# Kernel tuning notes

Hardware: AMD Instinct MI355X
Metric: run time of the kernel (lower is better)

The kernel has to match this reference:

```python
import jax, jax.numpy as jnp
import numpy as np

NUM_HEADS = 4
D_MODEL = 256
HEAD_DIM = D_MODEL // NUM_HEADS  # 64
B, N = 8, 2048


def _proj(x, W, b):
    # Conv1d with kernel_size=1 == pointwise linear over channel dim
    # x: [B, C_in, N], W: [C_out, C_in], b: [C_out]
    return jnp.einsum('oi,bin->bon', W, x) + b[None, :, None]


def setup_inputs() -> dict:
    key = jax.random.key(0)
    ks = jax.random.split(key, 11)
    s = 1.0 / np.sqrt(D_MODEL)
    return {
        'query': jax.random.normal(ks[0], (B, D_MODEL, N), jnp.float32),
        'key':   jax.random.normal(ks[1], (B, D_MODEL, N), jnp.float32),
        'value': jax.random.normal(ks[2], (B, D_MODEL, N), jnp.float32),
        'Wq': jax.random.normal(ks[3], (D_MODEL, D_MODEL), jnp.float32) * s,
        'bq': jax.random.normal(ks[4], (D_MODEL,), jnp.float32) * 0.01,
        'Wk': jax.random.normal(ks[5], (D_MODEL, D_MODEL), jnp.float32) * s,
        'bk': jax.random.normal(ks[6], (D_MODEL,), jnp.float32) * 0.01,
        'Wv': jax.random.normal(ks[7], (D_MODEL, D_MODEL), jnp.float32) * s,
        'bv': jax.random.normal(ks[8], (D_MODEL,), jnp.float32) * 0.01,
        'Wm': jax.random.normal(ks[9], (D_MODEL, D_MODEL), jnp.float32) * s,
        'bm': jax.random.normal(ks[10], (D_MODEL,), jnp.float32) * 0.01,
    }


def reference(query, key, value, Wq, bq, Wk, bk, Wv, bv, Wm, bm):
    b = query.shape[0]
    # project then split channels into (head_dim, num_heads): [B, d, h, N]
    q = _proj(query, Wq, bq).reshape(b, HEAD_DIM, NUM_HEADS, -1)
    k = _proj(key,   Wk, bk).reshape(b, HEAD_DIM, NUM_HEADS, -1)
    v = _proj(value, Wv, bv).reshape(b, HEAD_DIM, NUM_HEADS, -1)
    scale = 1.0 / jnp.sqrt(jnp.asarray(HEAD_DIM, q.dtype))
    scores = jnp.einsum('bdhn,bdhm->bhnm', q, k) * scale  # [B,H,N,N]
    prob = jax.nn.softmax(scores, axis=-1)
    x = jnp.einsum('bhnm,bdhm->bdhn', prob, v)  # [B,d,H,N]
    x = x.reshape(b, HEAD_DIM * NUM_HEADS, -1)  # [B, d_model, N]
    return _proj(x, Wm, bm)
```

## Files before the change

### kernel.cpp

```cpp
#include <hip/hip_runtime.h>
#include <math.h>


constexpr int BATCH  = 8;
constexpr int DMODEL = 256;
constexpr int SEQ    = 2048;
constexpr int HDIM   = 64;
constexpr int TN     = 128;
constexpr int TM     = 64;
constexpr int NJT    = SEQ / TM;

typedef _Float16 half4_t __attribute__((ext_vector_type(4)));
typedef _Float16 half8_t __attribute__((ext_vector_type(8)));
typedef float    float4_t __attribute__((ext_vector_type(4)));

static __device__ __forceinline__ void ld16_lds(const void* g, void* l) {
    __builtin_amdgcn_global_load_lds(
        (const __attribute__((address_space(1))) unsigned*)g,
        (__attribute__((address_space(3))) unsigned*)l, 16, 0, 0);
}

__global__ __launch_bounds__(256)
void prep_w(const float* __restrict__ Wq, const float* __restrict__ Wk,
            const float* __restrict__ Wv, const float* __restrict__ Wm,
            _Float16* __restrict__ wf)
{
    const int which = blockIdx.y;
    const float* src = which == 0 ? Wq : which == 1 ? Wk : which == 2 ? Wv : Wm;
    const int i = (blockIdx.x * 256 + threadIdx.x) * 4;
    const float4 v = *(const float4*)&src[i];
    half4_t o; o[0] = v.x; o[1] = v.y; o[2] = v.z; o[3] = v.w;
    *(half4_t*)&wf[(size_t)which * DMODEL * DMODEL + i] = o;
}

__global__ __launch_bounds__(256, 3)
void gemm_qkv(const _Float16* __restrict__ wf, const float* __restrict__ bq,
              const float* __restrict__ bk, const float* __restrict__ bv,
              const float* __restrict__ Xq, const float* __restrict__ Xk,
              const float* __restrict__ Xv, _Float16* __restrict__ qT,
              _Float16* __restrict__ kT, _Float16* __restrict__ vT)
{
    const int n0 = blockIdx.x * 64;
    const int proj = blockIdx.y >> 3, b = blockIdx.y & 7;
    const _Float16* W    = wf + (size_t)proj * DMODEL * DMODEL;
    const float*    bias = proj == 0 ? bq : proj == 1 ? bk : bv;
    const float*    X    = (proj == 0 ? Xq : proj == 1 ? Xk : Xv)
                           + (size_t)b * DMODEL * SEQ;

    __shared__ __align__(16) char lds[50432];
    float*    T  = (float*)lds;
    _Float16* Xs = (_Float16*)(lds + 16640);
    _Float16* Tw = (_Float16*)lds;

    const int tid = threadIdx.x, tn = tid & 15, tc = tid >> 4;

    #pragma unroll
    for (int cc = 0; cc < 4; ++cc) {
        __syncthreads();
        #pragma unroll
        for (int i = 0; i < 4; ++i) {
            const int c = tc + 16 * i;
            const float4 v = *(const float4*)&X[(size_t)(cc * 64 + c) * SEQ + n0 + tn * 4];
            T[c * 65 + tn * 4 + 0] = v.x; T[c * 65 + tn * 4 + 1] = v.y;
            T[c * 65 + tn * 4 + 2] = v.z; T[c * 65 + tn * 4 + 3] = v.w;
        }
        __syncthreads();
        #pragma unroll
        for (int i = 0; i < 4; ++i) {
            const int n = tc + 16 * i;
            half4_t h4;
            #pragma unroll
            for (int j = 0; j < 4; ++j) h4[j] = (_Float16)T[(tn * 4 + j) * 65 + n];
            *(half4_t*)&Xs[n * 264 + cc * 64 + tn * 4] = h4;
        }
    }
    __syncthreads();

    const int w = tid >> 6, lane = tid & 63;
    const int lm = lane & 15, g = lane >> 4, g8 = g * 8;
    const int cw0 = w * 64;

    float4_t acc[4][4];
    #pragma unroll
    for (int mt = 0; mt < 4; ++mt)
        #pragma unroll
        for (int nt = 0; nt < 4; ++nt) acc[mt][nt] = (float4_t){0.f, 0.f, 0.f, 0.f};

    #pragma unroll
    for (int k0 = 0; k0 < DMODEL; k0 += 64) {
        half8_t a[4][2], bb[4][2];
        #pragma unroll
        for (int mt = 0; mt < 4; ++mt)
            #pragma unroll
            for (int kd = 0; kd < 2; ++kd)
                a[mt][kd] = *(const half8_t*)&W[(size_t)(cw0 + mt * 16 + lm) * DMODEL
                                                + k0 + kd * 32 + g8];
        #pragma unroll
        for (int nt = 0; nt < 4; ++nt)
            #pragma unroll
            for (int kd = 0; kd < 2; ++kd)
                bb[nt][kd] = *(const half8_t*)&Xs[(nt * 16 + lm) * 264
                                                  + k0 + kd * 32 + g8];
        #pragma unroll
        for (int kd = 0; kd < 2; ++kd)
            #pragma unroll
            for (int mt = 0; mt < 4; ++mt)
                #pragma unroll
                for (int nt = 0; nt < 4; ++nt)
                    acc[mt][nt] = __builtin_amdgcn_mfma_f32_16x16x32_f16(
                        a[mt][kd], bb[nt][kd], acc[mt][nt], 0, 0, 0);
    }
    __syncthreads();

    #pragma unroll
    for (int mt = 0; mt < 4; ++mt) {
        const float4 b4 = *(const float4*)&bias[cw0 + mt * 16 + g * 4];
        const float bb4[4] = {b4.x, b4.y, b4.z, b4.w};
        #pragma unroll
        for (int nt = 0; nt < 4; ++nt) {
            half4_t pk;
            #pragma unroll
            for (int r = 0; r < 4; ++r) pk[r] = (_Float16)(acc[mt][nt][r] + bb4[r]);
            *(half4_t*)&Tw[((w * 64 + nt * 16 + lm)) * 68 + mt * 16 + g * 4] = pk;
        }
    }

    if (proj < 2) {
        _Float16* dst = (proj == 0 ? qT : kT);
        const int h2 = lane >> 4, lml = lane & 15;
        #pragma unroll
        for (int it = 0; it < 4; ++it) {
            const int nl = it * 16 + lml;
            #pragma unroll
            for (int dc = 0; dc < 2; ++dc) {
                half8_t ch;
                #pragma unroll
                for (int e = 0; e < 8; ++e)
                    ch[e] = Tw[(w * 64 + nl) * 68 + 4 * (dc * 8 + e) + h2];
                const int chunk = (w * 2 + dc) ^ (nl & 7);
                *(half8_t*)&dst[((size_t)(b * 4 + h2) * SEQ + n0 + nl) * HDIM
                                + chunk * 8] = ch;
            }
        }
    } else {
        const int hh = lane & 3, dl = (lane >> 2) & 15;
        const int d = w * 16 + dl;
        const size_t rowbase =
            (((size_t)(b * 4 + hh) * NJT + (n0 >> 6)) * HDIM + d) * (size_t)TM;
        #pragma unroll
        for (int jc = 0; jc < 8; ++jc) {
            half8_t ch;
            #pragma unroll
            for (int e = 0; e < 8; ++e)
                ch[e] = Tw[(w * 64 + jc * 8 + e) * 68 + 4 * dl + hh];
            *(half8_t*)&vT[rowbase + ((jc ^ (dl & 7)) << 3)] = ch;
        }
    }
}

__global__ __launch_bounds__(256, 4)
void attn_f16(const _Float16* __restrict__ qT, const _Float16* __restrict__ kT,
              const _Float16* __restrict__ vT, _Float16* __restrict__ xa,
              _Float16* __restrict__ xb, float* __restrict__ rs)
{
    const int bh = blockIdx.z, b = bh >> 2, h = bh & 3;
    const int jh = blockIdx.y;
    const int tid = threadIdx.x, wid = tid >> 6, lane = tid & 63;
    const int lm = lane & 15, g = lane >> 4;
    const int i0 = blockIdx.x * TN + wid * 32;

    __shared__ _Float16 Kb[2][TM * HDIM];
    __shared__ _Float16 Vb[2][TM * HDIM];

    half8_t bq[2][2];
    const _Float16* qbase = qT + (size_t)bh * SEQ * HDIM;
    #pragma unroll
    for (int rt = 0; rt < 2; ++rt)
        #pragma unroll
        for (int kd = 0; kd < 2; ++kd) {
            const int row = i0 + rt * 16 + lm;
            half8_t r8 = *(const half8_t*)(qbase + (size_t)row * HDIM
                                           + (((kd * 4 + g) ^ (lm & 7)) << 3));
            #pragma unroll
            for (int e = 0; e < 8; ++e) r8[e] = r8[e] * (_Float16)0.125f;
            bq[rt][kd] = r8;
        }

    const char* kt = (const char*)(kT + ((size_t)bh * SEQ + jh * (SEQ / 2)) * HDIM);
    const char* vt = (const char*)(vT + ((size_t)bh * NJT + jh * 16) * TM * HDIM);

    float4_t o[2][4], o5[2];
    #pragma unroll
    for (int rt = 0; rt < 2; ++rt) {
        #pragma unroll
        for (int dt = 0; dt < 4; ++dt) o[rt][dt] = (float4_t){0.f, 0.f, 0.f, 0.f};
        o5[rt] = (float4_t){0.f, 0.f, 0.f, 0.f};
    }
    const half4_t vone = {(_Float16)1.f, (_Float16)1.f, (_Float16)1.f, (_Float16)1.f};

    #define STAGE(jt, bu)                                                     \
        {                                                                     \
            const char* kg = kt + (size_t)(jt) * 8192;                        \
            const char* vg = vt + (size_t)(jt) * 8192;                        \
            _Pragma("unroll")                                                 \
            for (int p = 0; p < 2; ++p) {                                     \
                const int c = wid + p * 4;                                    \
                ld16_lds(kg + c * 1024 + lane * 16, (char*)&Kb[bu][0] + c * 1024); \
                ld16_lds(vg + c * 1024 + lane * 16, (char*)&Vb[bu][0] + c * 1024); \
            }                                                                 \
        }

    STAGE(0, 0);
    __syncthreads();

    for (int jt = 0; jt < 16; ++jt) {
        const int cur = jt & 1;
        if (jt + 1 < 16) STAGE(jt + 1, cur ^ 1);

        float4_t s[4][2];
        #pragma unroll
        for (int ct = 0; ct < 4; ++ct)
            #pragma unroll
            for (int rt = 0; rt < 2; ++rt) s[ct][rt] = (float4_t){0.f, 0.f, 0.f, 0.f};
        #pragma unroll
        for (int kd = 0; kd < 2; ++kd)
            #pragma unroll
            for (int ct = 0; ct < 4; ++ct) {
                const half8_t fk = *(const half8_t*)
                    &Kb[cur][(ct * 16 + lm) * HDIM + (((kd * 4 + g) ^ (lm & 7)) << 3)];
                #pragma unroll
                for (int rt = 0; rt < 2; ++rt)
                    s[ct][rt] = __builtin_amdgcn_mfma_f32_16x16x32_f16(
                        fk, bq[rt][kd], s[ct][rt], 0, 0, 0);
            }

        half4_t ap[4][2];
        #pragma unroll
        for (int ct = 0; ct < 4; ++ct)
            #pragma unroll
            for (int rt = 0; rt < 2; ++rt)
                #pragma unroll
                for (int r = 0; r < 4; ++r)
                    ap[ct][rt][r] = (_Float16)__expf(s[ct][rt][r]);
        #pragma unroll
        for (int ct = 0; ct < 4; ++ct)
            #pragma unroll
            for (int rt = 0; rt < 2; ++rt)
                o5[rt] = __builtin_amdgcn_mfma_f32_16x16x16f16(
                    ap[ct][rt], vone, o5[rt], 0, 0, 0);

        #pragma unroll
        for (int ct = 0; ct < 4; ++ct)
            #pragma unroll
            for (int dt = 0; dt < 4; ++dt) {
                const int d = dt * 16 + lm;
                const half4_t fv = *(const half4_t*)
                    &Vb[cur][d * TM + ((((ct * 2 + (g >> 1)) ^ (lm & 7)) << 3)
                                       + ((g & 1) << 2))];
                #pragma unroll
                for (int rt = 0; rt < 2; ++rt)
                    o[rt][dt] = __builtin_amdgcn_mfma_f32_16x16x16f16(
                        ap[ct][rt], fv, o[rt][dt], 0, 0, 0);
            }
        __syncthreads();
    }

    _Float16* xp = jh ? xb : xa;
    #pragma unroll
    for (int rt = 0; rt < 2; ++rt)
        #pragma unroll
        for (int dt = 0; dt < 4; ++dt) {
            const int c = 4 * (dt * 16 + lm) + h;
            #pragma unroll
            for (int r = 0; r < 4; ++r) {
                const int n = i0 + rt * 16 + 4 * g + r;
                xp[((size_t)b * SEQ + n) * DMODEL + c] = (_Float16)o[rt][dt][r];
            }
        }
    if (lm == 0) {
        #pragma unroll
        for (int rt = 0; rt < 2; ++rt)
            #pragma unroll
            for (int r = 0; r < 4; ++r)
                rs[((size_t)jh * 32 + bh) * SEQ + i0 + rt * 16 + 4 * g + r] =
                    o5[rt][r];
    }
    #undef STAGE
}

__global__ __launch_bounds__(256)
void gemm_final(const _Float16* __restrict__ wm, const float* __restrict__ bias,
                const _Float16* __restrict__ xa, const _Float16* __restrict__ xb,
                const float* __restrict__ rs, float* __restrict__ out)
{
    const int n0 = blockIdx.x * 64, m0 = blockIdx.y * 128;
    const int b = blockIdx.z;
    const int tid = threadIdx.x, w = tid >> 6, lane = tid & 63;
    const int lm = lane & 15, g = lane >> 4, g8 = g * 8;
    const int cw0 = m0 + w * 32;

    const _Float16* Xa = xa + ((size_t)b * SEQ + n0) * DMODEL;
    const _Float16* Xb2 = xb + ((size_t)b * SEQ + n0) * DMODEL;

    half8_t pm[4];
    #pragma unroll
    for (int nt = 0; nt < 4; ++nt) {
        const int n = n0 + nt * 16 + lm;
        #pragma unroll
        for (int hh = 0; hh < 4; ++hh) {
            const float l = rs[(size_t)(b * 4 + hh) * SEQ + n]
                          + rs[(size_t)(32 + b * 4 + hh) * SEQ + n];
            const _Float16 iv = (_Float16)(1.0f / l);
            pm[nt][hh] = iv; pm[nt][hh + 4] = iv;
        }
    }

    float4_t acc[2][4];
    #pragma unroll
    for (int mt = 0; mt < 2; ++mt)
        #pragma unroll
        for (int nt = 0; nt < 4; ++nt) acc[mt][nt] = (float4_t){0.f, 0.f, 0.f, 0.f};

    #pragma unroll
    for (int k0 = 0; k0 < DMODEL; k0 += 64) {
        half8_t a[2][2], bb[4][2];
        #pragma unroll
        for (int mt = 0; mt < 2; ++mt)
            #pragma unroll
            for (int kd = 0; kd < 2; ++kd)
                a[mt][kd] = *(const half8_t*)&wm[(size_t)(cw0 + mt * 16 + lm) * DMODEL
                                                 + k0 + kd * 32 + g8];
        #pragma unroll
        for (int nt = 0; nt < 4; ++nt)
            #pragma unroll
            for (int kd = 0; kd < 2; ++kd) {
                const size_t off = (size_t)(nt * 16 + lm) * DMODEL + k0 + kd * 32 + g8;
                const half8_t va = *(const half8_t*)&Xa[off];
                const half8_t vb = *(const half8_t*)&Xb2[off];
                bb[nt][kd] = (va + vb) * pm[nt];
            }
        #pragma unroll
        for (int kd = 0; kd < 2; ++kd)
            #pragma unroll
            for (int mt = 0; mt < 2; ++mt)
                #pragma unroll
                for (int nt = 0; nt < 4; ++nt)
                    acc[mt][nt] = __builtin_amdgcn_mfma_f32_16x16x32_f16(
                        a[mt][kd], bb[nt][kd], acc[mt][nt], 0, 0, 0);
    }

    #pragma unroll
    for (int mt = 0; mt < 2; ++mt)
        #pragma unroll
        for (int r = 0; r < 4; ++r) {
            const int co = cw0 + mt * 16 + g * 4 + r;
            const float bv_ = bias[co];
            #pragma unroll
            for (int nt = 0; nt < 4; ++nt)
                out[((size_t)b * DMODEL + co) * SEQ + n0 + nt * 16 + lm] =
                    acc[mt][nt][r] + bv_;
        }
}

extern "C" void kernel_launch(void* const* d_in, const int* in_sizes, int n_in,
                              void* d_out, int out_size, void* d_ws, size_t ws_size,
                              hipStream_t stream) {
    const float* query = (const float*)d_in[0];
    const float* key_  = (const float*)d_in[1];
    const float* value = (const float*)d_in[2];
    const float* Wq = (const float*)d_in[3];  const float* bq = (const float*)d_in[4];
    const float* Wk = (const float*)d_in[5];  const float* bk = (const float*)d_in[6];
    const float* Wv = (const float*)d_in[7];  const float* bv = (const float*)d_in[8];
    const float* Wm = (const float*)d_in[9];  const float* bm = (const float*)d_in[10];
    float* out = (float*)d_out;

    const size_t bufElems = (size_t)BATCH * DMODEL * SEQ;
    _Float16* qT = (_Float16*)d_ws;
    _Float16* kT = qT + bufElems;
    _Float16* vT = kT + bufElems;
    _Float16* xa = vT + bufElems;
    _Float16* xb = xa + bufElems;
    _Float16* wf = xb + bufElems;
    float*    rsb = (float*)(wf + 4 * DMODEL * DMODEL);

    prep_w<<<dim3(DMODEL * DMODEL / 1024, 4), 256, 0, stream>>>(Wq, Wk, Wv, Wm, wf);
    gemm_qkv<<<dim3(SEQ / 64, 3 * BATCH), 256, 0, stream>>>(
        wf, bq, bk, bv, query, key_, value, qT, kT, vT);
    attn_f16<<<dim3(SEQ / TN, 2, BATCH * 4), 256, 0, stream>>>(qT, kT, vT, xa, xb, rsb);
    gemm_final<<<dim3(SEQ / 64, 2, BATCH), 256, 0, stream>>>(
        wf + (size_t)3 * DMODEL * DMODEL, bm, xa, xb, rsb, out);
}
```

Measured before the change: 197.3 us.

## Fold softmax scale into Q projection, use exp2, scalar row sums, remap grid

The Q projection epilogue now multiplies by 0.125*log2(e), so the attention kernel can drop its per-load Q scaling and call the hardware exp2 directly. The row-sum MFMA against a ones vector is replaced by scalar accumulation plus two cross-lane shuffles. The V tile layout gets an extra half-swizzle to reduce LDS bank conflicts. The 3D grid becomes a 1D grid remapped so the 8 XCDs share K/V data. Folding the scale into fp16 Q changes rounding slightly, and the swizzle must stay consistent between writer and reader.

```diff
diff --git a/kernel.cpp b/kernel.cpp
--- a/kernel.cpp
+++ b/kernel.cpp
@@ -46,6 +46,7 @@
     const float*    bias = proj == 0 ? bq : proj == 1 ? bk : bv;
     const float*    X    = (proj == 0 ? Xq : proj == 1 ? Xk : Xv)
                            + (size_t)b * DMODEL * SEQ;
+    const float qs = (proj == 0) ? 0.18033688011112042f : 1.0f;
 
     __shared__ __align__(16) char lds[50432];
     float*    T  = (float*)lds;
@@ -120,7 +121,8 @@
         for (int nt = 0; nt < 4; ++nt) {
             half4_t pk;
             #pragma unroll
-            for (int r = 0; r < 4; ++r) pk[r] = (_Float16)(acc[mt][nt][r] + bb4[r]);
+            for (int r = 0; r < 4; ++r)
+                pk[r] = (_Float16)((acc[mt][nt][r] + bb4[r]) * qs);
             *(half4_t*)&Tw[((w * 64 + nt * 16 + lm)) * 68 + mt * 16 + g * 4] = pk;
         }
     }
@@ -145,6 +147,7 @@
     } else {
         const int hh = lane & 3, dl = (lane >> 2) & 15;
         const int d = w * 16 + dl;
+        const int hswap = ((dl >> 3) & 1) << 2;
         const size_t rowbase =
             (((size_t)(b * 4 + hh) * NJT + (n0 >> 6)) * HDIM + d) * (size_t)TM;
         #pragma unroll
@@ -152,7 +155,7 @@
             half8_t ch;
             #pragma unroll
             for (int e = 0; e < 8; ++e)
-                ch[e] = Tw[(w * 64 + jc * 8 + e) * 68 + 4 * dl + hh];
+                ch[e] = Tw[(w * 64 + jc * 8 + (e ^ hswap)) * 68 + 4 * dl + hh];
             *(half8_t*)&vT[rowbase + ((jc ^ (dl & 7)) << 3)] = ch;
         }
     }
@@ -163,11 +166,14 @@
               const _Float16* __restrict__ vT, _Float16* __restrict__ xa,
               _Float16* __restrict__ xb, float* __restrict__ rs)
 {
-    const int bh = blockIdx.z, b = bh >> 2, h = bh & 3;
-    const int jh = blockIdx.y;
+    const int lid = blockIdx.x;
+    const int work = (lid & 7) * 128 + (lid >> 3);
+    const int bh = work >> 5, b = bh >> 2, h = bh & 3;
+    const int jh = (work >> 4) & 1;
+    const int ib = work & 15;
     const int tid = threadIdx.x, wid = tid >> 6, lane = tid & 63;
     const int lm = lane & 15, g = lane >> 4;
-    const int i0 = blockIdx.x * TN + wid * 32;
+    const int i0 = ib * TN + wid * 32;
 
     __shared__ _Float16 Kb[2][TM * HDIM];
     __shared__ _Float16 Vb[2][TM * HDIM];
@@ -179,24 +185,19 @@
         #pragma unroll
         for (int kd = 0; kd < 2; ++kd) {
             const int row = i0 + rt * 16 + lm;
-            half8_t r8 = *(const half8_t*)(qbase + (size_t)row * HDIM
+            bq[rt][kd] = *(const half8_t*)(qbase + (size_t)row * HDIM
                                            + (((kd * 4 + g) ^ (lm & 7)) << 3));
-            #pragma unroll
-            for (int e = 0; e < 8; ++e) r8[e] = r8[e] * (_Float16)0.125f;
-            bq[rt][kd] = r8;
         }
 
     const char* kt = (const char*)(kT + ((size_t)bh * SEQ + jh * (SEQ / 2)) * HDIM);
     const char* vt = (const char*)(vT + ((size_t)bh * NJT + jh * 16) * TM * HDIM);
 
-    float4_t o[2][4], o5[2];
-    #pragma unroll
-    for (int rt = 0; rt < 2; ++rt) {
+    float4_t o[2][4];
+    float rsum[2] = {0.f, 0.f};
+    #pragma unroll
+    for (int rt = 0; rt < 2; ++rt)
         #pragma unroll
         for (int dt = 0; dt < 4; ++dt) o[rt][dt] = (float4_t){0.f, 0.f, 0.f, 0.f};
-        o5[rt] = (float4_t){0.f, 0.f, 0.f, 0.f};
-    }
-    const half4_t vone = {(_Float16)1.f, (_Float16)1.f, (_Float16)1.f, (_Float16)1.f};
 
     #define STAGE(jt, bu)                                                     \
         {                                                                     \
@@ -240,14 +241,11 @@
             #pragma unroll
             for (int rt = 0; rt < 2; ++rt)
                 #pragma unroll
-                for (int r = 0; r < 4; ++r)
-                    ap[ct][rt][r] = (_Float16)__expf(s[ct][rt][r]);
-        #pragma unroll
-        for (int ct = 0; ct < 4; ++ct)
-            #pragma unroll
-            for (int rt = 0; rt < 2; ++rt)
-                o5[rt] = __builtin_amdgcn_mfma_f32_16x16x16f16(
-                    ap[ct][rt], vone, o5[rt], 0, 0, 0);
+                for (int r = 0; r < 4; ++r) {
+                    const float e = __builtin_amdgcn_exp2f(s[ct][rt][r]);
+                    rsum[rt] += e;
+                    ap[ct][rt][r] = (_Float16)e;
+                }
 
         #pragma unroll
         for (int ct = 0; ct < 4; ++ct)
@@ -256,7 +254,7 @@
                 const int d = dt * 16 + lm;
                 const half4_t fv = *(const half4_t*)
                     &Vb[cur][d * TM + ((((ct * 2 + (g >> 1)) ^ (lm & 7)) << 3)
-                                       + ((g & 1) << 2))];
+                                       + (((g & 1) ^ (lm >> 3)) << 2))];
                 #pragma unroll
                 for (int rt = 0; rt < 2; ++rt)
                     o[rt][dt] = __builtin_amdgcn_mfma_f32_16x16x16f16(
@@ -277,13 +275,13 @@
                 xp[((size_t)b * SEQ + n) * DMODEL + c] = (_Float16)o[rt][dt][r];
             }
         }
-    if (lm == 0) {
-        #pragma unroll
-        for (int rt = 0; rt < 2; ++rt)
-            #pragma unroll
-            for (int r = 0; r < 4; ++r)
-                rs[((size_t)jh * 32 + bh) * SEQ + i0 + rt * 16 + 4 * g + r] =
-                    o5[rt][r];
+    #pragma unroll
+    for (int rt = 0; rt < 2; ++rt) {
+        float v = rsum[rt];
+        v += __shfl_xor(v, 16);
+        v += __shfl_xor(v, 32);
+        if (g == 0)
+            rs[((size_t)jh * 32 + bh) * SEQ + i0 + rt * 16 + lm] = v;
     }
     #undef STAGE
 }
@@ -386,7 +384,7 @@
     prep_w<<<dim3(DMODEL * DMODEL / 1024, 4), 256, 0, stream>>>(Wq, Wk, Wv, Wm, wf);
     gemm_qkv<<<dim3(SEQ / 64, 3 * BATCH), 256, 0, stream>>>(
         wf, bq, bk, bv, query, key_, value, qT, kT, vT);
-    attn_f16<<<dim3(SEQ / TN, 2, BATCH * 4), 256, 0, stream>>>(qT, kT, vT, xa, xb, rsb);
+    attn_f16<<<dim3(1024), 256, 0, stream>>>(qT, kT, vT, xa, xb, rsb);
     gemm_final<<<dim3(SEQ / 64, 2, BATCH), 256, 0, stream>>>(
         wf + (size_t)3 * DMODEL * DMODEL, bm, xa, xb, rsb, out);
 }
```

After: 191.1 us. -3.2%, faster.
